# Kernel tuning notes

Hardware: AMD Instinct MI355X
Metric: run time of the kernel (lower is better)

The kernel has to match this reference:

```python
import jax, jax.numpy as jnp
import numpy as np

B, S, D_MODEL, NUM_HEADS, MAX_LEN = 4, 1024, 1024, 16, 1024
D_HEAD = D_MODEL // NUM_HEADS


def _skew(QEr):
    # QEr: (b, h, s, s). Music-Transformer skew: pad one col on the left,
    # reshape swapping the last two dims, drop the first row.
    b, h, r, c = QEr.shape
    padded = jnp.pad(QEr, ((0, 0), (0, 0), (0, 0), (1, 0)))  # (b,h,r,c+1)
    reshaped = padded.reshape(b, h, c + 1, r)
    return reshaped[:, :, 1:, :]  # (b,h,s,s)


def setup_inputs() -> dict:
    key = jax.random.key(0)
    ks = jax.random.split(key, 8)
    sc = 1.0 / np.sqrt(D_MODEL).astype(np.float32)
    return {
        "x": jax.random.normal(ks[0], (B, S, D_MODEL), jnp.float32),
        "Wq": jax.random.normal(ks[1], (D_MODEL, D_MODEL), jnp.float32) * sc,
        "bq": jnp.zeros((D_MODEL,), jnp.float32),
        "Wk": jax.random.normal(ks[2], (D_MODEL, D_MODEL), jnp.float32) * sc,
        "bk": jnp.zeros((D_MODEL,), jnp.float32),
        "Wv": jax.random.normal(ks[3], (D_MODEL, D_MODEL), jnp.float32) * sc,
        "bv": jnp.zeros((D_MODEL,), jnp.float32),
        "Er": jax.random.normal(ks[4], (MAX_LEN, D_HEAD), jnp.float32),
    }


def reference(x, Wq, bq, Wk, bk, Wv, bv, Er):
    b, s, _ = x.shape
    h, dh = NUM_HEADS, D_HEAD
    # projections -> (b, h, s, dh). Weights stored [in, out] (equiv. to torch W.T).
    q = (x @ Wq + bq).reshape(b, s, h, dh).transpose(0, 2, 1, 3)
    k = (x @ Wk + bk).reshape(b, s, h, dh).transpose(0, 2, 1, 3)
    v = (x @ Wv + bv).reshape(b, s, h, dh).transpose(0, 2, 1, 3)
    Er_t = Er[MAX_LEN - s:, :]                      # (s, dh)
    QEr = jnp.einsum('bhsd,td->bhst', q, Er_t)      # (b,h,s,s)
    Srel = _skew(QEr)
    scores = (jnp.einsum('bhsd,bhtd->bhst', q, k) + Srel) / np.float32(np.sqrt(dh))
    causal = jnp.tril(jnp.ones((s, s), bool))       # (s,s)
    scores = jnp.where(causal[None, None], scores, -jnp.inf)
    attn = jax.nn.softmax(scores, axis=-1)
    out = jnp.einsum('bhst,bhtd->bhsd', attn, v)    # (b,h,s,dh)
    return out.transpose(0, 2, 1, 3).reshape(b, s, h * dh)
```

## Files before the change

kernel.cpp:

```cpp
#include <hip/hip_runtime.h>
#include <hip/hip_bf16.h>
#include <math.h>

typedef __attribute__((ext_vector_type(8))) short short8;
typedef __attribute__((ext_vector_type(4))) float f32x4;
typedef __attribute__((ext_vector_type(4))) unsigned short us4;
typedef __attribute__((ext_vector_type(2))) unsigned int u32x2;

#define DM 1024
#define NH 16
#define DH 64
#define SS 1024
#define C2 0.180336879f

#define GLDS16(g, l) __builtin_amdgcn_global_load_lds(                      \
    (const __attribute__((address_space(1))) unsigned int*)(g),             \
    (__attribute__((address_space(3))) unsigned int*)(l), 16, 0, 0)

__device__ __forceinline__ unsigned short f2b(float f){
    unsigned int u = __float_as_uint(f);
    u += 0x7fffu + ((u >> 16) & 1u);
    return (unsigned short)(u >> 16);
}
__device__ __forceinline__ float b2f(unsigned short b){
    return __uint_as_float(((unsigned int)b) << 16);
}
__device__ __forceinline__ unsigned int cvt_pk_bf16(float lo, float hi){
    unsigned int r;
    asm volatile("v_cvt_pk_bf16_f32 %0, %1, %2" : "=v"(r) : "v"(lo), "v"(hi));
    return r;
}

__global__ __launch_bounds__(256) void cast_f32_bf16_k(const float* __restrict__ in,
                                                       unsigned short* __restrict__ out){
    int i = (blockIdx.x * 256 + threadIdx.x) * 4;
    float4 v = *(const float4*)(in + i);
    us4 o = { f2b(v.x), f2b(v.y), f2b(v.z), f2b(v.w) };
    *(us4*)(out + i) = o;
}

__global__ __launch_bounds__(256) void transpose_cast_w_k(const float* __restrict__ Wq,
                                                          const float* __restrict__ Wk,
                                                          const float* __restrict__ Wv,
                                                          unsigned short* __restrict__ wT){
    __shared__ float tile[32][33];
    const float* W = blockIdx.z==0 ? Wq : (blockIdx.z==1 ? Wk : Wv);
    int o0 = blockIdx.x*32, k0 = blockIdx.y*32;
    int tx = threadIdx.x, ty = threadIdx.y;
    #pragma unroll
    for (int i=0;i<32;i+=8) tile[ty+i][tx] = W[(k0+ty+i)*DM + o0+tx];
    __syncthreads();
    #pragma unroll
    for (int i=0;i<32;i+=8) wT[(blockIdx.z*DM + o0+ty+i)*DM + k0+tx] = f2b(tile[tx][ty+i]);
}

__global__ __launch_bounds__(256) void gemm_qkv_k(
    const unsigned short* __restrict__ xb, const unsigned short* __restrict__ wT,
    const float* __restrict__ bq, const float* __restrict__ bk, const float* __restrict__ bv,
    unsigned short* __restrict__ Qb, unsigned short* __restrict__ Kb, unsigned short* __restrict__ VTb)
{
    __shared__ unsigned short smem[2*128*64];
    unsigned short* lda = smem;
    unsigned short* ldb = smem + 128*64;
    const int tid = threadIdx.x;
    const int lane = tid & 63, w = tid >> 6;
    const int wr = w >> 1, wc = w & 1;
    const int lr = lane & 15, lk4 = lane >> 4;
    const int m0 = blockIdx.y * 128, n0 = blockIdx.x * 128;
    f32x4 acc[4][4] = {};
    for (int k0 = 0; k0 < DM; k0 += 64){
        #pragma unroll
        for (int p=0;p<4;p++){
            int idx = tid + p*256;
            int row = idx >> 3, ch = idx & 7;
            GLDS16(&xb[(m0+row)*DM + k0 + ((ch ^ (row&7))<<3)], &lda[idx<<3]);
            GLDS16(&wT[(n0+row)*DM + k0 + ((ch ^ (row&7))<<3)], &ldb[idx<<3]);
        }
        __syncthreads();
        #pragma unroll
        for (int kk=0;kk<2;kk++){
            const int sco = ((kk*4+lk4) ^ (lr&7)) << 3;
            short8 a[4], b[4];
            #pragma unroll
            for (int m=0;m<4;m++) a[m] = *(const short8*)(&lda[(wr*64+m*16+lr)*64 + sco]);
            #pragma unroll
            for (int n=0;n<4;n++) b[n] = *(const short8*)(&ldb[(wc*64+n*16+lr)*64 + sco]);
            __builtin_amdgcn_s_setprio(1);
            #pragma unroll
            for (int m=0;m<4;m++)
                #pragma unroll
                for (int n=0;n<4;n++)
                    acc[m][n] = __builtin_amdgcn_mfma_f32_16x16x32_bf16(a[m], b[n], acc[m][n], 0,0,0);
            __builtin_amdgcn_s_setprio(0);
        }
        __syncthreads();
    }
    if (n0 < 2048){
        #pragma unroll
        for (int m=0;m<4;m++){
            #pragma unroll
            for (int n=0;n<4;n++){
                int C = n0 + wc*64 + n*16 + lr;
                int proj = C >> 10, hd = C & 1023;
                float badd = (proj==0 ? bq : bk)[hd];
                int h = hd >> 6, d = hd & 63;
                #pragma unroll
                for (int r=0;r<4;r++){
                    int R = m0 + wr*64 + m*16 + lk4*4 + r;
                    int b_ = R >> 10, s = R & 1023;
                    float v = acc[m][n][r] + badd;
                    (proj==0 ? Qb : Kb)[(((b_*NH)+h)*SS + s)*DH + d] = f2b(proj==0 ? v*C2 : v);
                }
            }
        }
    } else {
        char* tb = (char*)smem;
        #pragma unroll
        for (int n=0;n<4;n++){
            int Cl = wc*64 + n*16 + lr;
            float badd = bv[n0 - 2048 + Cl];
            #pragma unroll
            for (int m=0;m<4;m++){
                int R0 = wr*64 + m*16 + lk4*4;
                us4 pk = { f2b(acc[m][n][0] + badd), f2b(acc[m][n][1] + badd),
                           f2b(acc[m][n][2] + badd), f2b(acc[m][n][3] + badd) };
                *(us4*)(tb + (Cl<<8) + (((R0<<1)) ^ ((Cl&7)<<4))) = pk;
            }
        }
        __syncthreads();
        const int b_ = m0 >> 10;
        const int sres = m0 & 1023;
        #pragma unroll
        for (int q=0;q<8;q++){
            int idx = q*256 + tid;
            int dl = idx >> 4;
            int sc = idx & 15;
            short8 o = *(const short8*)(tb + (dl<<8) + (((sc<<4)) ^ ((dl&7)<<4)));
            int Cg = n0 - 2048 + dl;
            int h = Cg >> 6, d = Cg & 63;
            *(short8*)(&VTb[(((b_*NH)+h)*DH + d)*SS + sres + sc*8]) = o;
        }
    }
}

__global__ __launch_bounds__(256) void attn_k(
    const unsigned short* __restrict__ Qb, const unsigned short* __restrict__ Kb,
    const unsigned short* __restrict__ VTb, const unsigned short* __restrict__ Erb,
    float* __restrict__ out)
{
    __shared__ unsigned short k_lds[64*64];
    __shared__ unsigned short vt_lds[64*64];
    __shared__ unsigned short er_lds[128*64];
    __shared__ unsigned short p_lds[64*64];
    __shared__ unsigned short rbt[4][80*20];

    const int tid = threadIdx.x, lane = tid & 63, w = tid >> 6;
    const int lr = lane & 15, lk4 = lane >> 4;
    const int bh = blockIdx.x;
    const int pr = blockIdx.y;
    const unsigned short* q_b  = Qb  + bh*SS*DH;
    const unsigned short* k_b  = Kb  + bh*SS*DH;
    const unsigned short* vt_b = VTb + bh*DH*SS;

    auto STAGE_K = [&](int j0){
        #pragma unroll
        for (int p=0;p<2;p++){
            int idx = tid + p*256;
            int row = idx >> 3, ch = idx & 7;
            GLDS16(&k_b[(j0+row)*DH + ((ch ^ (row&7))<<3)], &k_lds[idx<<3]);
        }
    };
    auto STAGE_VT = [&](int j0){
        #pragma unroll
        for (int p=0;p<2;p++){
            int idx = tid + p*256;
            int row = idx >> 3, ch = idx & 7;
            GLDS16(&vt_b[row*SS + j0 + ((ch ^ (row&7))<<3)], &vt_lds[idx<<3]);
        }
    };
    auto STAGE_ER = [&](int t0){
        #pragma unroll
        for (int p=0;p<4;p++){
            int idx = tid + p*256;
            int row = idx >> 3, ch = idx & 7;
            GLDS16(&Erb[(t0+row)*DH + ((ch ^ (row&7))<<3)], &er_lds[idx<<3]);
        }
    };

    unsigned short* rbw = &rbt[w][0];
    const int fbase = 3 - w;

    for (int seg=0; seg<2; ++seg){
        const int ib = seg ? 15 - pr : pr;
        const int i0 = ib * 64;
        const int ntiles = ib + 1;

        STAGE_K(0);
        STAGE_ER(960 - i0);

        short8 qf[2];
        #pragma unroll
        for (int kk=0;kk<2;kk++)
            qf[kk] = *(const short8*)(&q_b[(i0 + w*16 + lr)*DH + kk*32 + lk4*8]);

        __syncthreads();

        f32x4 o_acc[4] = {};
        float l_r[4] = {0.f,0.f,0.f,0.f};

        for (int t=0; t<ntiles; t++){
            const int j0 = t*64;
            STAGE_VT(j0);

            f32x4 s_acc[4] = {};
            f32x4 r_acc[5] = {};
            __builtin_amdgcn_s_setprio(1);
            #pragma unroll
            for (int kk=0;kk<2;kk++){
                const int sco = ((kk*4+lk4) ^ (lr&7)) << 3;
                #pragma unroll
                for (int n=0;n<4;n++){
                    short8 kf = *(const short8*)(&k_lds[(n*16+lr)*64 + sco]);
                    s_acc[n] = __builtin_amdgcn_mfma_f32_16x16x32_bf16(qf[kk], kf, s_acc[n], 0,0,0);
                }
                #pragma unroll
                for (int fi=0;fi<5;fi++){
                    short8 ef = *(const short8*)(&er_lds[((fbase+fi)*16+lr)*64 + sco]);
                    r_acc[fi] = __builtin_amdgcn_mfma_f32_16x16x32_bf16(qf[kk], ef, r_acc[fi], 0,0,0);
                }
            }
            __builtin_amdgcn_s_setprio(0);

            __syncthreads();
            if (t+1 < ntiles){
                STAGE_K(j0+64);
                STAGE_ER(960 - i0 + j0 + 64);
            }

            #pragma unroll
            for (int fi=0;fi<5;fi++){
                u32x2 pk;
                pk[0] = cvt_pk_bf16(r_acc[fi][0], r_acc[fi][1]);
                pk[1] = cvt_pk_bf16(r_acc[fi][2], r_acc[fi][3]);
                *(u32x2*)(&rbw[(fi*16+lr)*20 + lk4*4]) = pk;
            }

            float s2[4][4];
            #pragma unroll
            for (int r=0;r<4;r++){
                const int rr = lk4*4 + r;
                const int gb = (15 - rr + lr)*20 + rr;
                #pragma unroll
                for (int n=0;n<4;n++)
                    s2[n][r] = s_acc[n][r] + b2f(rbw[gb + n*320]);
            }
            if (t == ntiles-1){
                #pragma unroll
                for (int r=0;r<4;r++){
                    const int gi = i0 + w*16 + lk4*4 + r;
                    #pragma unroll
                    for (int n=0;n<4;n++)
                        if (j0 + n*16 + lr > gi) s2[n][r] = -INFINITY;
                }
            }
            #pragma unroll
            for (int r=0;r<4;r++){
                float p0 = __builtin_amdgcn_exp2f(s2[0][r]);
                float p1 = __builtin_amdgcn_exp2f(s2[1][r]);
                float p2 = __builtin_amdgcn_exp2f(s2[2][r]);
                float p3 = __builtin_amdgcn_exp2f(s2[3][r]);
                l_r[r] += (p0+p1)+(p2+p3);
                unsigned int u01 = cvt_pk_bf16(p0, p1);
                unsigned int u23 = cvt_pk_bf16(p2, p3);
                const int li = w*16 + lk4*4 + r;
                const int ro = li*64 + (lr&7);
                p_lds[ro + (((0 + (lr>>3)) ^ (li&7))<<3)] = (unsigned short)u01;
                p_lds[ro + (((2 + (lr>>3)) ^ (li&7))<<3)] = (unsigned short)(u01>>16);
                p_lds[ro + (((4 + (lr>>3)) ^ (li&7))<<3)] = (unsigned short)u23;
                p_lds[ro + (((6 + (lr>>3)) ^ (li&7))<<3)] = (unsigned short)(u23>>16);
            }

            __builtin_amdgcn_s_setprio(1);
            #pragma unroll
            for (int kk=0;kk<2;kk++){
                const int sco = ((kk*4+lk4) ^ (lr&7)) << 3;
                short8 pf = *(const short8*)(&p_lds[(w*16+lr)*64 + sco]);
                #pragma unroll
                for (int n=0;n<4;n++){
                    short8 vf = *(const short8*)(&vt_lds[(n*16+lr)*64 + sco]);
                    o_acc[n] = __builtin_amdgcn_mfma_f32_16x16x32_bf16(pf, vf, o_acc[n], 0,0,0);
                }
            }
            __builtin_amdgcn_s_setprio(0);
            __syncthreads();
        }

        #pragma unroll
        for (int r=0;r<4;r++){
            float l = l_r[r];
            #pragma unroll
            for (int msk=1; msk<16; msk<<=1) l += __shfl_xor(l, msk);
            l_r[r] = 1.0f / l;
        }
        const int b_ = bh >> 4, h = bh & 15;
        #pragma unroll
        for (int n=0;n<4;n++)
            #pragma unroll
            for (int r=0;r<4;r++){
                int li = w*16 + lk4*4 + r;
                int d = n*16 + lr;
                out[(b_*SS + i0 + li)*DM + h*DH + d] = o_acc[n][r] * l_r[r];
            }
    }
}

extern "C" void kernel_launch(void* const* d_in, const int* in_sizes, int n_in,
                              void* d_out, int out_size, void* d_ws, size_t ws_size,
                              hipStream_t stream)
{
    const float* x  = (const float*)d_in[0];
    const float* Wq = (const float*)d_in[1];
    const float* bq = (const float*)d_in[2];
    const float* Wk = (const float*)d_in[3];
    const float* bk = (const float*)d_in[4];
    const float* Wv = (const float*)d_in[5];
    const float* bv = (const float*)d_in[6];
    const float* Er = (const float*)d_in[7];
    float* out = (float*)d_out;
    char* ws = (char*)d_ws;
    unsigned short* xb  = (unsigned short*)(ws);
    unsigned short* wT  = (unsigned short*)(ws + 8388608);
    unsigned short* erb = (unsigned short*)(ws + 14680064);
    unsigned short* Qb  = (unsigned short*)(ws + 14827520);
    unsigned short* Kb  = (unsigned short*)(ws + 23216128);
    unsigned short* VTb = (unsigned short*)(ws + 31604736);

    cast_f32_bf16_k<<<4096, 256, 0, stream>>>(x, xb);
    cast_f32_bf16_k<<<64, 256, 0, stream>>>(Er, erb);
    hipMemsetAsync(erb + 1024*DH, 0, 128*DH*sizeof(unsigned short), stream);
    transpose_cast_w_k<<<dim3(32,32,3), dim3(32,8), 0, stream>>>(Wq, Wk, Wv, wT);
    gemm_qkv_k<<<dim3(24,32), 256, 0, stream>>>(xb, wT, bq, bk, bv, Qb, Kb, VTb);
    attn_k<<<dim3(64,8), 256, 0, stream>>>(Qb, Kb, VTb, erb, out);
}
```

Measured before the change: 93.51 us.

## Split V projection into transposed GEMM and stage only new Er half per tile

Splits the fused QKV GEMM into a Q/K GEMM and a separate V GEMM that computes V^T directly by swapping operands, so the LDS transpose and extra sync in the epilogue go away. The V^T epilogue now writes scattered 2-byte stores instead of vectorised 16-byte stores, and it adds one extra kernel launch. In the attention kernel, the Er window is handled as a 128-row ring buffer. Each tile loads only the 64 new rows instead of reloading all 128, which halves the Er staging traffic.

```diff
diff --git a/kernel.cpp b/kernel.cpp
--- a/kernel.cpp
+++ b/kernel.cpp
@@ -54,14 +54,13 @@
     for (int i=0;i<32;i+=8) wT[(blockIdx.z*DM + o0+ty+i)*DM + k0+tx] = f2b(tile[tx][ty+i]);
 }
 
-__global__ __launch_bounds__(256) void gemm_qkv_k(
+__global__ __launch_bounds__(256) void gemm_qk_k(
     const unsigned short* __restrict__ xb, const unsigned short* __restrict__ wT,
-    const float* __restrict__ bq, const float* __restrict__ bk, const float* __restrict__ bv,
-    unsigned short* __restrict__ Qb, unsigned short* __restrict__ Kb, unsigned short* __restrict__ VTb)
+    const float* __restrict__ bq, const float* __restrict__ bk,
+    unsigned short* __restrict__ Qb, unsigned short* __restrict__ Kb)
 {
-    __shared__ unsigned short smem[2*128*64];
-    unsigned short* lda = smem;
-    unsigned short* ldb = smem + 128*64;
+    __shared__ unsigned short lda[128*64];
+    __shared__ unsigned short ldb[128*64];
     const int tid = threadIdx.x;
     const int lane = tid & 63, w = tid >> 6;
     const int wr = w >> 1, wc = w & 1;
@@ -95,50 +94,77 @@
         }
         __syncthreads();
     }
-    if (n0 < 2048){
-        #pragma unroll
-        for (int m=0;m<4;m++){
-            #pragma unroll
-            for (int n=0;n<4;n++){
-                int C = n0 + wc*64 + n*16 + lr;
-                int proj = C >> 10, hd = C & 1023;
-                float badd = (proj==0 ? bq : bk)[hd];
-                int h = hd >> 6, d = hd & 63;
-                #pragma unroll
-                for (int r=0;r<4;r++){
-                    int R = m0 + wr*64 + m*16 + lk4*4 + r;
-                    int b_ = R >> 10, s = R & 1023;
-                    float v = acc[m][n][r] + badd;
-                    (proj==0 ? Qb : Kb)[(((b_*NH)+h)*SS + s)*DH + d] = f2b(proj==0 ? v*C2 : v);
-                }
-            }
-        }
-    } else {
-        char* tb = (char*)smem;
+    #pragma unroll
+    for (int m=0;m<4;m++){
         #pragma unroll
         for (int n=0;n<4;n++){
-            int Cl = wc*64 + n*16 + lr;
-            float badd = bv[n0 - 2048 + Cl];
-            #pragma unroll
-            for (int m=0;m<4;m++){
-                int R0 = wr*64 + m*16 + lk4*4;
-                us4 pk = { f2b(acc[m][n][0] + badd), f2b(acc[m][n][1] + badd),
-                           f2b(acc[m][n][2] + badd), f2b(acc[m][n][3] + badd) };
-                *(us4*)(tb + (Cl<<8) + (((R0<<1)) ^ ((Cl&7)<<4))) = pk;
-            }
-        }
-        __syncthreads();
-        const int b_ = m0 >> 10;
-        const int sres = m0 & 1023;
-        #pragma unroll
-        for (int q=0;q<8;q++){
-            int idx = q*256 + tid;
-            int dl = idx >> 4;
-            int sc = idx & 15;
-            short8 o = *(const short8*)(tb + (dl<<8) + (((sc<<4)) ^ ((dl&7)<<4)));
-            int Cg = n0 - 2048 + dl;
-            int h = Cg >> 6, d = Cg & 63;
-            *(short8*)(&VTb[(((b_*NH)+h)*DH + d)*SS + sres + sc*8]) = o;
+            int C = n0 + wc*64 + n*16 + lr;
+            int proj = C >> 10, hd = C & 1023;
+            float badd = (proj==0 ? bq : bk)[hd];
+            int h = hd >> 6, d = hd & 63;
+            #pragma unroll
+            for (int r=0;r<4;r++){
+                int R = m0 + wr*64 + m*16 + lk4*4 + r;
+                int b_ = R >> 10, s = R & 1023;
+                float v = acc[m][n][r] + badd;
+                (proj==0 ? Qb : Kb)[(((b_*NH)+h)*SS + s)*DH + d] = f2b(proj==0 ? v*C2 : v);
+            }
+        }
+    }
+}
+
+__global__ __launch_bounds__(256) void gemm_vt_k(
+    const unsigned short* __restrict__ xb, const unsigned short* __restrict__ wTv,
+    const float* __restrict__ bv, unsigned short* __restrict__ VTb)
+{
+    __shared__ unsigned short lda[128*64];
+    __shared__ unsigned short ldb[128*64];
+    const int tid = threadIdx.x;
+    const int lane = tid & 63, w = tid >> 6;
+    const int wr = w >> 1, wc = w & 1;
+    const int lr = lane & 15, lk4 = lane >> 4;
+    const int o0 = blockIdx.x * 128;
+    const int s0 = blockIdx.y * 128;
+    f32x4 acc[4][4] = {};
+    for (int k0 = 0; k0 < DM; k0 += 64){
+        #pragma unroll
+        for (int p=0;p<4;p++){
+            int idx = tid + p*256;
+            int row = idx >> 3, ch = idx & 7;
+            GLDS16(&wTv[(o0+row)*DM + k0 + ((ch ^ (row&7))<<3)], &lda[idx<<3]);
+            GLDS16(&xb[(s0+row)*DM + k0 + ((ch ^ (row&7))<<3)], &ldb[idx<<3]);
+        }
+        __syncthreads();
+        #pragma unroll
+        for (int kk=0;kk<2;kk++){
+            const int sco = ((kk*4+lk4) ^ (lr&7)) << 3;
+            short8 a[4], b[4];
+            #pragma unroll
+            for (int m=0;m<4;m++) a[m] = *(const short8*)(&lda[(wr*64+m*16+lr)*64 + sco]);
+            #pragma unroll
+            for (int n=0;n<4;n++) b[n] = *(const short8*)(&ldb[(wc*64+n*16+lr)*64 + sco]);
+            __builtin_amdgcn_s_setprio(1);
+            #pragma unroll
+            for (int m=0;m<4;m++)
+                #pragma unroll
+                for (int n=0;n<4;n++)
+                    acc[m][n] = __builtin_amdgcn_mfma_f32_16x16x32_bf16(a[m], b[n], acc[m][n], 0,0,0);
+            __builtin_amdgcn_s_setprio(0);
+        }
+        __syncthreads();
+    }
+    #pragma unroll
+    for (int m=0;m<4;m++){
+        #pragma unroll
+        for (int n=0;n<4;n++){
+            int sg = s0 + wc*64 + n*16 + lr;
+            int b_ = sg >> 10, s = sg & 1023;
+            #pragma unroll
+            for (int r=0;r<4;r++){
+                int o = o0 + wr*64 + m*16 + lk4*4 + r;
+                int h = o >> 6, d = o & 63;
+                VTb[(((b_*NH)+h)*DH + d)*SS + s] = f2b(acc[m][n][r] + bv[o]);
+            }
         }
     }
 }
@@ -178,12 +204,21 @@
             GLDS16(&vt_b[row*SS + j0 + ((ch ^ (row&7))<<3)], &vt_lds[idx<<3]);
         }
     };
-    auto STAGE_ER = [&](int t0){
+    auto STAGE_ER_FULL = [&](int t0){
         #pragma unroll
         for (int p=0;p<4;p++){
             int idx = tid + p*256;
             int row = idx >> 3, ch = idx & 7;
             GLDS16(&Erb[(t0+row)*DH + ((ch ^ (row&7))<<3)], &er_lds[idx<<3]);
+        }
+    };
+    auto STAGE_ER_HALF = [&](int absbase, int rof){
+        #pragma unroll
+        for (int p=0;p<2;p++){
+            int idx = tid + p*256;
+            int q = idx >> 3, ch = idx & 7;
+            GLDS16(&Erb[(absbase+q)*DH + ((ch ^ (q&7))<<3)],
+                   &er_lds[((((q+rof)<<3) + ch))<<3]);
         }
     };
 
@@ -194,9 +229,10 @@
         const int ib = seg ? 15 - pr : pr;
         const int i0 = ib * 64;
         const int ntiles = ib + 1;
+        const int t0s = 960 - i0;
 
         STAGE_K(0);
-        STAGE_ER(960 - i0);
+        STAGE_ER_FULL(t0s);
 
         short8 qf[2];
         #pragma unroll
@@ -210,6 +246,7 @@
 
         for (int t=0; t<ntiles; t++){
             const int j0 = t*64;
+            const int rof = (t & 1) * 64;
             STAGE_VT(j0);
 
             f32x4 s_acc[4] = {};
@@ -225,7 +262,8 @@
                 }
                 #pragma unroll
                 for (int fi=0;fi<5;fi++){
-                    short8 ef = *(const short8*)(&er_lds[((fbase+fi)*16+lr)*64 + sco]);
+                    const int ero = (((fbase+fi)*16+lr) + rof) & 127;
+                    short8 ef = *(const short8*)(&er_lds[ero*64 + sco]);
                     r_acc[fi] = __builtin_amdgcn_mfma_f32_16x16x32_bf16(qf[kk], ef, r_acc[fi], 0,0,0);
                 }
             }
@@ -234,7 +272,7 @@
             __syncthreads();
             if (t+1 < ntiles){
                 STAGE_K(j0+64);
-                STAGE_ER(960 - i0 + j0 + 64);
+                STAGE_ER_HALF(t0s + j0 + 128, rof);
             }
 
             #pragma unroll
@@ -339,6 +377,7 @@
     cast_f32_bf16_k<<<64, 256, 0, stream>>>(Er, erb);
     hipMemsetAsync(erb + 1024*DH, 0, 128*DH*sizeof(unsigned short), stream);
     transpose_cast_w_k<<<dim3(32,32,3), dim3(32,8), 0, stream>>>(Wq, Wk, Wv, wT);
-    gemm_qkv_k<<<dim3(24,32), 256, 0, stream>>>(xb, wT, bq, bk, bv, Qb, Kb, VTb);
+    gemm_qk_k<<<dim3(16,32), 256, 0, stream>>>(xb, wT, bq, bk, Qb, Kb);
+    gemm_vt_k<<<dim3(8,32), 256, 0, stream>>>(xb, wT + 2048*DM, bv, VTb);
     attn_k<<<dim3(64,8), 256, 0, stream>>>(Qb, Kb, VTb, erb, out);
 }
```

Measured after the change: 98.33 us. 5.2% more time.
